# Kernel optimization log

Hardware: AMD Instinct MI355X
Metric: run time of the kernel (lower is better)

The kernel has to match this reference:

```python
import jax, jax.numpy as jnp
import numpy as np

# db4 filter bank (matches pywt.Wavelet('db4'))
_F = 8
_h = np.array([-0.010597401784997278, 0.032883011666982945, 0.030841381835986965,
               -0.18703481171888114, -0.02798376941698385, 0.6308807679295904,
               0.7148465705525415, 0.23037781330885523], dtype=np.float32)  # dec_lo
_sgn = ((-1.0) ** np.arange(_F)).astype(np.float32)
DEC_LO = jnp.asarray(_h)
DEC_HI = jnp.asarray(-_sgn * _h[::-1])          # dec_hi[k] = (-1)^(k+1) dec_lo[F-1-k]
REC_LO = jnp.asarray(_h[::-1].copy())
REC_HI = jnp.asarray(_sgn * _h)
LEVEL = 4


def _dwt(x):
    # x: [B, n] -> (cA, cD) each [B, floor((n+F-1)/2)]; pywt symmetric mode:
    # out[i] = sum_k h[k] * xe[2i + F - k], xe = symmetric-extended signal.
    xe = jnp.pad(x, ((0, 0), (_F - 1, _F - 1)), mode='symmetric')[:, 1:]
    k = jnp.stack([DEC_LO[::-1], DEC_HI[::-1]])[:, None, :]  # [2, 1, F]
    y = jax.lax.conv_general_dilated(xe[:, None, :], k, (2,), 'VALID')
    return y[:, 0], y[:, 1]


def _idwt(ca, cd):
    # pywt idwt: full conv of zero-upsampled coeffs with rec filters,
    # slice [F-2 : 2n] -> output length 2n - F + 2.
    n = ca.shape[1]
    u = jnp.stack([ca, cd], axis=1)                             # [B, 2, n]
    k = jnp.stack([REC_LO[::-1], REC_HI[::-1]])[None, :, :]     # [1, 2, F]
    y = jax.lax.conv_general_dilated(u, k, (1,), [(_F - 1, _F - 1)], lhs_dilation=(2,))
    return y[:, 0, _F - 2: 2 * n]


def _wavedec(x):
    a = x
    details = []
    for _ in range(LEVEL):
        a, d = _dwt(a)
        details.append(d)
    return [a] + details[::-1]  # [cA_L, cD_L, ..., cD_1]


def _waverec(coeffs):
    a = coeffs[0]
    for d in coeffs[1:]:
        if a.shape[1] == d.shape[1] + 1:  # pywt waverec length-fixup
            a = a[:, :-1]
        a = _idwt(a, d)
    return a


def setup_inputs() -> dict:
    key = jax.random.key(0)
    x = jax.random.normal(key, (4096, 1, 5000), dtype=jnp.float32)
    return {"x": x}


def reference(x):
    # x: [B, 1, L]. Returns (physio, identity), each [B, 1, L].
    n = x.shape[2]
    coeffs = _wavedec(x[:, 0, :])
    zeros = [jnp.zeros_like(c) for c in coeffs]
    physio = _waverec(coeffs[:3] + zeros[3:])[:, :n]    # cA_4, cD_4, cD_3 kept
    identity = _waverec(zeros[:3] + coeffs[3:])[:, :n]  # cD_2, cD_1 kept
    return physio[:, None, :], identity[:, None, :]
```

## Files before the change

kernel.cpp:

```cpp
#include <hip/hip_runtime.h>

#define NTHR 512
#define NROW 5000
#define NB1 2503
#define NB2 1255
#define NB3 631
#define NB4 319

__device__ __constant__ float DEC_LO[8] = {
    -0.010597401784997278f, 0.032883011666982945f, 0.030841381835986965f,
    -0.18703481171888114f, -0.02798376941698385f, 0.6308807679295904f,
    0.7148465705525415f, 0.23037781330885523f};
__device__ __constant__ float DEC_HI[8] = {
    -0.23037781330885523f, 0.7148465705525415f, -0.6308807679295904f,
    -0.02798376941698385f, 0.18703481171888114f, 0.030841381835986965f,
    -0.032883011666982945f, -0.010597401784997278f};
__device__ __constant__ float REC_LO[8] = {
    0.23037781330885523f, 0.7148465705525415f, 0.6308807679295904f,
    -0.02798376941698385f, -0.18703481171888114f, 0.030841381835986965f,
    0.032883011666982945f, -0.010597401784997278f};
__device__ __constant__ float REC_HI[8] = {
    -0.010597401784997278f, -0.032883011666982945f, 0.030841381835986965f,
    0.18703481171888114f, -0.02798376941698385f, -0.6308807679295904f,
    0.7148465705525415f, -0.23037781330885523f};

__device__ __forceinline__ void dwt_accum2(const float v[10], float& sa0, float& sd0,
                                           float& sa1, float& sd1) {
  sa0 = sd0 = sa1 = sd1 = 0.f;
#pragma unroll
  for (int j = 0; j < 8; ++j) {
    const float lo = DEC_LO[7 - j], hi = DEC_HI[7 - j];
    sa0 = fmaf(lo, v[j], sa0);
    sd0 = fmaf(hi, v[j], sd0);
    sa1 = fmaf(lo, v[j + 2], sa1);
    sd1 = fmaf(hi, v[j + 2], sd1);
  }
}

__device__ __forceinline__ void dwt_glob(const float* __restrict__ x, int n, int n_out,
                                         float* __restrict__ oa, float* __restrict__ od,
                                         int tid) {
  const int npair = (n_out + 1) / 2;
  for (int t = tid; t < npair; t += NTHR) {
    const int i0 = 2 * t;
    float v[10];
    if (i0 >= 3 && 2 * i0 + 4 <= n) {
      const float2* s2 = reinterpret_cast<const float2*>(x + 2 * i0 - 6);
#pragma unroll
      for (int j = 0; j < 5; ++j) {
        const float2 p = s2[j];
        v[2 * j] = p.x;
        v[2 * j + 1] = p.y;
      }
    } else {
#pragma unroll
      for (int j = 0; j < 10; ++j) {
        const int p = 2 * i0 + j;
        const int q = (p < 6) ? (5 - p) : ((p < n + 6) ? (p - 6) : (2 * n + 5 - p));
        v[j] = x[q];
      }
    }
    float sa0, sd0, sa1, sd1;
    dwt_accum2(v, sa0, sd0, sa1, sd1);
    if (i0 + 1 < n_out) {
      *reinterpret_cast<float2*>(oa + i0) = make_float2(sa0, sa1);
      *reinterpret_cast<float2*>(od + i0) = make_float2(sd0, sd1);
    } else {
      oa[i0] = sa0;
      od[i0] = sd0;
    }
  }
}

__device__ __forceinline__ void dwt_step(const float* __restrict__ src, int n, int n_out,
                                         float* __restrict__ oa, float* __restrict__ od,
                                         int tid) {
  const int npair = (n_out + 1) / 2;
  for (int t = tid; t < npair; t += NTHR) {
    const int i0 = 2 * t;
    float v[10];
    if (i0 >= 3 && 2 * i0 + 4 <= n) {
      const float2* s2 = reinterpret_cast<const float2*>(src + 2 * i0 - 6);
#pragma unroll
      for (int j = 0; j < 5; ++j) {
        const float2 p = s2[j];
        v[2 * j] = p.x;
        v[2 * j + 1] = p.y;
      }
    } else {
#pragma unroll
      for (int j = 0; j < 10; ++j) {
        const int p = 2 * i0 + j;
        const int q = (p < 6) ? (5 - p) : ((p < n + 6) ? (p - 6) : (2 * n + 5 - p));
        v[j] = src[q];
      }
    }
    float sa0, sd0, sa1, sd1;
    dwt_accum2(v, sa0, sd0, sa1, sd1);
    if (i0 + 1 < n_out) {
      *reinterpret_cast<float2*>(oa + i0) = make_float2(sa0, sa1);
      *reinterpret_cast<float2*>(od + i0) = make_float2(sd0, sd1);
    } else {
      oa[i0] = sa0;
      od[i0] = sd0;
    }
  }
}

template <bool CA, bool CD>
__device__ __forceinline__ void idwt_pair(const float* __restrict__ ca,
                                          const float* __restrict__ cd, int i0,
                                          float4& r) {
  float a[5], d[5];
  if (CA) {
    const float2 u0 = *reinterpret_cast<const float2*>(ca + i0);
    const float2 u1 = *reinterpret_cast<const float2*>(ca + i0 + 2);
    a[0] = u0.x; a[1] = u0.y; a[2] = u1.x; a[3] = u1.y; a[4] = ca[i0 + 4];
  }
  if (CD) {
    const float2 w0 = *reinterpret_cast<const float2*>(cd + i0);
    const float2 w1 = *reinterpret_cast<const float2*>(cd + i0 + 2);
    d[0] = w0.x; d[1] = w0.y; d[2] = w1.x; d[3] = w1.y; d[4] = cd[i0 + 4];
  }
  float e0 = 0.f, o0 = 0.f, e1 = 0.f, o1 = 0.f;
#pragma unroll
  for (int s = 0; s < 4; ++s) {
    const float rl0 = REC_LO[2 * s], rl1 = REC_LO[2 * s + 1];
    const float rh0 = REC_HI[2 * s], rh1 = REC_HI[2 * s + 1];
    if (CA) {
      e0 = fmaf(rl0, a[3 - s], e0);
      o0 = fmaf(rl1, a[3 - s], o0);
      e1 = fmaf(rl0, a[4 - s], e1);
      o1 = fmaf(rl1, a[4 - s], o1);
    }
    if (CD) {
      e0 = fmaf(rh0, d[3 - s], e0);
      o0 = fmaf(rh1, d[3 - s], o0);
      e1 = fmaf(rh0, d[4 - s], e1);
      o1 = fmaf(rh1, d[4 - s], o1);
    }
  }
  r = make_float4(e0, o0, e1, o1);
}

template <bool CA, bool CD>
__device__ __forceinline__ void idwt_any(const float* __restrict__ ca,
                                         const float* __restrict__ cd, int n,
                                         float* __restrict__ out, int tid) {
  const int npair = (n - 3) / 2;
  float4* out4 = reinterpret_cast<float4*>(out);
  for (int t = tid; t < npair; t += NTHR) {
    float4 r;
    idwt_pair<CA, CD>(ca, cd, 2 * t, r);
    out4[t] = r;
  }
}

__global__ __launch_bounds__(NTHR, 8) void wavelet_kernel(
    const float* __restrict__ x, float* __restrict__ out_physio,
    float* __restrict__ out_identity) {
  __shared__ __align__(16) float A[2504];
  __shared__ __align__(16) float B[2504];
  __shared__ __align__(16) float C[1256];
  __shared__ __align__(16) float D[1256];

  float* const a3 = A;
  float* const d3 = A + 632;
  float* const a4 = A + 1264;
  float* const d4 = A + 1584;

  const int b = blockIdx.x;
  const int tid = threadIdx.x;
  const float* xrow = x + (size_t)b * NROW;

  dwt_glob(xrow, NROW, NB1, A, B, tid);
  __syncthreads();
  dwt_step(A, NB1, NB2, C, D, tid);
  __syncthreads();
  dwt_step(C, NB2, NB3, a3, d3, tid);
  __syncthreads();
  dwt_step(a3, NB3, NB4, a4, d4, tid);
  __syncthreads();

  idwt_any<true, true>(a4, d4, NB4, A, tid);
  __syncthreads();
  idwt_any<true, true>(A, d3, NB3, C, tid);
  __syncthreads();
  idwt_any<true, false>(C, nullptr, NB2, A, tid);
  __syncthreads();
  idwt_any<true, false>(A, nullptr, NB1, out_physio + (size_t)b * NROW, tid);
  __syncthreads();

  idwt_any<false, true>(nullptr, D, NB2, A, tid);
  __syncthreads();
  idwt_any<true, true>(A, B, NB1, out_identity + (size_t)b * NROW, tid);
}

extern "C" void kernel_launch(void* const* d_in, const int* in_sizes, int n_in,
                              void* d_out, int out_size, void* d_ws, size_t ws_size,
                              hipStream_t stream) {
  const float* x = (const float*)d_in[0];
  float* out = (float*)d_out;
  const int B = in_sizes[0] / NROW;
  wavelet_kernel<<<dim3(B), dim3(NTHR), 0, stream>>>(x, out, out + (size_t)B * NROW);
}
```

Measured before the change: 47.74 us.

## Fuse pairs of inverse wavelet levels in registers to cut syncs and LDS traffic

Two consecutive IDWT levels are computed per thread in registers: level-4 plus level-3 reconstruction go into one pass, and the final two levels of both the physio and identity outputs are fused so each thread emits two float4s. This drops four barriers and the intermediate shared-memory round trips. In exchange, each thread recomputes overlapping upsampled values and uses more registers, and the physio and identity tails now run back-to-back without a barrier between them.

Result: slower. 57.19 us (+19.8%).

```diff
diff --git a/kernel.cpp b/kernel.cpp
--- a/kernel.cpp
+++ b/kernel.cpp
@@ -6,6 +6,10 @@
 #define NB2 1255
 #define NB3 631
 #define NB4 319
+
+#define NQ_PHYS 625
+#define NQ_IDEN 625
+#define NQ_R2 157
 
 __device__ __constant__ float DEC_LO[8] = {
     -0.010597401784997278f, 0.032883011666982945f, 0.030841381835986965f,
@@ -24,6 +28,7 @@
     0.18703481171888114f, -0.02798376941698385f, -0.6308807679295904f,
     0.7148465705525415f, -0.23037781330885523f};
 
+
 __device__ __forceinline__ void dwt_accum2(const float v[10], float& sa0, float& sd0,
                                            float& sa1, float& sd1) {
   sa0 = sd0 = sa1 = sd1 = 0.f;
@@ -107,21 +112,64 @@
   }
 }
 
+
+__device__ __forceinline__ void load7(const float* __restrict__ p, float w[7]) {
+  const float2 w0 = *reinterpret_cast<const float2*>(p);
+  const float2 w1 = *reinterpret_cast<const float2*>(p + 2);
+  const float2 w2 = *reinterpret_cast<const float2*>(p + 4);
+  w[0] = w0.x; w[1] = w0.y; w[2] = w1.x; w[3] = w1.y; w[4] = w2.x; w[5] = w2.y;
+  w[6] = p[6];
+}
+
+__device__ __forceinline__ void up_lo(const float w[7], float r[8]) {
+#pragma unroll
+  for (int k = 0; k < 4; ++k) {
+    float e = 0.f, o = 0.f;
+#pragma unroll
+    for (int s = 0; s < 4; ++s) {
+      const float c = w[k + 3 - s];
+      e = fmaf(REC_LO[2 * s], c, e);
+      o = fmaf(REC_LO[2 * s + 1], c, o);
+    }
+    r[2 * k] = e;
+    r[2 * k + 1] = o;
+  }
+}
+
+__device__ __forceinline__ void up_hi(const float w[7], float r[8]) {
+#pragma unroll
+  for (int k = 0; k < 4; ++k) {
+    float e = 0.f, o = 0.f;
+#pragma unroll
+    for (int s = 0; s < 4; ++s) {
+      const float c = w[k + 3 - s];
+      e = fmaf(REC_HI[2 * s], c, e);
+      o = fmaf(REC_HI[2 * s + 1], c, o);
+    }
+    r[2 * k] = e;
+    r[2 * k + 1] = o;
+  }
+}
+
+__device__ __forceinline__ void up_both(const float wa[7], const float wd[7], float r[8]) {
+#pragma unroll
+  for (int k = 0; k < 4; ++k) {
+    float e = 0.f, o = 0.f;
+#pragma unroll
+    for (int s = 0; s < 4; ++s) {
+      const float a = wa[k + 3 - s], d = wd[k + 3 - s];
+      e = fmaf(REC_LO[2 * s], a, e);
+      o = fmaf(REC_LO[2 * s + 1], a, o);
+      e = fmaf(REC_HI[2 * s], d, e);
+      o = fmaf(REC_HI[2 * s + 1], d, o);
+    }
+    r[2 * k] = e;
+    r[2 * k + 1] = o;
+  }
+}
+
 template <bool CA, bool CD>
-__device__ __forceinline__ void idwt_pair(const float* __restrict__ ca,
-                                          const float* __restrict__ cd, int i0,
-                                          float4& r) {
-  float a[5], d[5];
-  if (CA) {
-    const float2 u0 = *reinterpret_cast<const float2*>(ca + i0);
-    const float2 u1 = *reinterpret_cast<const float2*>(ca + i0 + 2);
-    a[0] = u0.x; a[1] = u0.y; a[2] = u1.x; a[3] = u1.y; a[4] = ca[i0 + 4];
-  }
-  if (CD) {
-    const float2 w0 = *reinterpret_cast<const float2*>(cd + i0);
-    const float2 w1 = *reinterpret_cast<const float2*>(cd + i0 + 2);
-    d[0] = w0.x; d[1] = w0.y; d[2] = w1.x; d[3] = w1.y; d[4] = cd[i0 + 4];
-  }
+__device__ __forceinline__ float4 pair_eo(const float* a, const float* d) {
   float e0 = 0.f, o0 = 0.f, e1 = 0.f, o1 = 0.f;
 #pragma unroll
   for (int s = 0; s < 4; ++s) {
@@ -140,19 +188,51 @@
       o1 = fmaf(rh1, d[4 - s], o1);
     }
   }
-  r = make_float4(e0, o0, e1, o1);
-}
-
-template <bool CA, bool CD>
-__device__ __forceinline__ void idwt_any(const float* __restrict__ ca,
-                                         const float* __restrict__ cd, int n,
-                                         float* __restrict__ out, int tid) {
-  const int npair = (n - 3) / 2;
+  return make_float4(e0, o0, e1, o1);
+}
+
+__device__ __forceinline__ void r2_fused(const float* __restrict__ a4,
+                                         const float* __restrict__ d4,
+                                         const float* __restrict__ d3,
+                                         float* __restrict__ r2out, int tid) {
+  float4* out4 = reinterpret_cast<float4*>(r2out);
+  for (int t = tid; t < NQ_R2; t += NTHR) {
+    float wa[7], wd[7], w3[7];
+    load7(a4 + 2 * t, wa);
+    load7(d4 + 2 * t, wd);
+    load7(d3 + 4 * t, w3);
+    float r3v[8];
+    up_both(wa, wd, r3v);
+    out4[2 * t] = pair_eo<true, true>(r3v, w3);
+    out4[2 * t + 1] = pair_eo<true, true>(r3v + 2, w3 + 2);
+  }
+}
+
+__device__ __forceinline__ void physio_fused(const float* __restrict__ r2,
+                                             float* __restrict__ out, int tid) {
   float4* out4 = reinterpret_cast<float4*>(out);
-  for (int t = tid; t < npair; t += NTHR) {
-    float4 r;
-    idwt_pair<CA, CD>(ca, cd, 2 * t, r);
-    out4[t] = r;
+  for (int t = tid; t < NQ_PHYS; t += NTHR) {
+    float w[7];
+    load7(r2 + 2 * t, w);
+    float r1v[8];
+    up_lo(w, r1v);
+    out4[2 * t] = pair_eo<true, false>(r1v, nullptr);
+    out4[2 * t + 1] = pair_eo<true, false>(r1v + 2, nullptr);
+  }
+}
+
+__device__ __forceinline__ void identity_fused(const float* __restrict__ d2,
+                                               const float* __restrict__ d1,
+                                               float* __restrict__ out, int tid) {
+  float4* out4 = reinterpret_cast<float4*>(out);
+  for (int t = tid; t < NQ_IDEN; t += NTHR) {
+    float w2[7], w1[7];
+    load7(d2 + 2 * t, w2);
+    load7(d1 + 4 * t, w1);
+    float s1v[8];
+    up_hi(w2, s1v);
+    out4[2 * t] = pair_eo<true, true>(s1v, w1);
+    out4[2 * t + 1] = pair_eo<true, true>(s1v + 2, w1 + 2);
   }
 }
 
@@ -182,18 +262,10 @@
   dwt_step(a3, NB3, NB4, a4, d4, tid);
   __syncthreads();
 
-  idwt_any<true, true>(a4, d4, NB4, A, tid);
-  __syncthreads();
-  idwt_any<true, true>(A, d3, NB3, C, tid);
-  __syncthreads();
-  idwt_any<true, false>(C, nullptr, NB2, A, tid);
-  __syncthreads();
-  idwt_any<true, false>(A, nullptr, NB1, out_physio + (size_t)b * NROW, tid);
-  __syncthreads();
-
-  idwt_any<false, true>(nullptr, D, NB2, A, tid);
-  __syncthreads();
-  idwt_any<true, true>(A, B, NB1, out_identity + (size_t)b * NROW, tid);
+  r2_fused(a4, d4, d3, C, tid);
+  __syncthreads();
+  physio_fused(C, out_physio + (size_t)b * NROW, tid);
+  identity_fused(D, B, out_identity + (size_t)b * NROW, tid);
 }
 
 extern "C" void kernel_launch(void* const* d_in, const int* in_sizes, int n_in,
```
